# Kernel optimization log

Hardware: AMD Instinct MI355X
Metric: run time of the kernel (lower is better)

The kernel has to match this reference:

```python
import jax, jax.numpy as jnp
import numpy as np

# dims
B, N, L = 8, 128, 512          # batch, n_vars, context_window
PL, ST = 16, 8                  # patch_len, stride
PN = (L - PL) // ST + 1         # patch_num = 63
DM, H, DFF, NL = 128, 16, 256, 2
DK = DM // H
DG, MP, BETA = 8, 3, 0.05       # d_gcn, mp_layers, propbeta
TW = 96                         # target_window


def setup_inputs() -> dict:
    key = jax.random.key(0)
    ks = iter(jax.random.split(key, 64))
    def nrm(shape, s=0.02):
        return jax.random.normal(next(ks), shape, jnp.float32) * s
    inp = {
        "x": jax.random.normal(next(ks), (B, N, L), jnp.float32),
        "adj_logits": jax.random.normal(next(ks), (B, L, N, N), jnp.float32),
        # DGCN params
        "dgcn_start_w": nrm((1, DG)), "dgcn_start_b": jnp.zeros((DG,), jnp.float32),
        "dgcn_mlp_w": nrm(((MP + 1) * DG, 1)), "dgcn_mlp_b": jnp.zeros((1,), jnp.float32),
        # patch embedding + positional
        "W_P": nrm((PL, DM)), "b_P": jnp.zeros((DM,), jnp.float32), "W_pos": nrm((PN, DM)),
        # encoder layers (stacked over NL)
        "Wq": nrm((NL, DM, DM)), "bq": jnp.zeros((NL, DM), jnp.float32),
        "Wk": nrm((NL, DM, DM)), "bk": jnp.zeros((NL, DM), jnp.float32),
        "Wv": nrm((NL, DM, DM)), "bv": jnp.zeros((NL, DM), jnp.float32),
        "Wo": nrm((NL, DM, DM)), "bo": jnp.zeros((NL, DM), jnp.float32),
        "scale": jnp.full((NL,), DK ** -0.5, jnp.float32),
        "bn1_g": jnp.ones((NL, DM), jnp.float32), "bn1_b": jnp.zeros((NL, DM), jnp.float32),
        "ff_w1": nrm((NL, DM, DFF)), "ff_b1": jnp.zeros((NL, DFF), jnp.float32),
        "ff_w2": nrm((NL, DFF, DM)), "ff_b2": jnp.zeros((NL, DM), jnp.float32),
        "bn2_g": jnp.ones((NL, DM), jnp.float32), "bn2_b": jnp.zeros((NL, DM), jnp.float32),
        # head
        "head_w": nrm((DM * PN, TW)), "head_b": jnp.zeros((TW,), jnp.float32),
    }
    return inp


def _bn(x, g, b):
    # BatchNorm1d in training mode over (batch, seq) per feature channel
    mu = x.mean(axis=(0, 1))
    var = x.var(axis=(0, 1))
    return (x - mu) * jax.lax.rsqrt(var + 1e-5) * g + b


def reference(x, adj_logits, dgcn_start_w, dgcn_start_b, dgcn_mlp_w, dgcn_mlp_b,
              W_P, b_P, W_pos, Wq, bq, Wk, bk, Wv, bv, Wo, bo, scale,
              bn1_g, bn1_b, ff_w1, ff_b1, ff_w2, ff_b2, bn2_g, bn2_b,
              head_w, head_b):
    # ---- DGCN: multi-hop diffusion over variables, per time step ----
    x4 = x[..., None]                                   # [b,n,s,1]
    A = jax.nn.softmax(adj_logits, axis=2)              # [b,s,n,m], normalized over source n
    a = jnp.transpose(A, (0, 2, 3, 1))                  # [b,n,m,s]
    h = x4 @ dgcn_start_w + dgcn_start_b                # [b,n,s,d_gcn]
    outs = [h]
    for _ in range(MP):
        h = BETA * x4 + (1.0 - BETA) * jnp.einsum('bnsc,bnms->bmsc', h, a)
        outs.append(h)
    y = (jnp.concatenate(outs, axis=-1) @ dgcn_mlp_w + dgcn_mlp_b)[..., 0]  # [b,n,s]
    # ---- patching ----
    win = jnp.arange(PN)[:, None] * ST + jnp.arange(PL)[None, :]
    z = y[:, :, win]                                    # [b,n,pn,pl]
    # ---- TSTiEncoder (channel independent) ----
    src = (z @ W_P + b_P).reshape(B * N, PN, DM) + W_pos
    prev = None
    for l in range(NL):
        q = (src @ Wq[l] + bq[l]).reshape(-1, PN, H, DK).transpose(0, 2, 1, 3)
        k = (src @ Wk[l] + bk[l]).reshape(-1, PN, H, DK).transpose(0, 2, 1, 3)
        v = (src @ Wv[l] + bv[l]).reshape(-1, PN, H, DK).transpose(0, 2, 1, 3)
        scores = jnp.einsum('bhqd,bhkd->bhqk', q, k) * scale[l]
        if prev is not None:
            scores = scores + prev                      # residual attention
        w = jax.nn.softmax(scores, axis=-1)
        o = jnp.einsum('bhqk,bhkd->bhqd', w, v).transpose(0, 2, 1, 3).reshape(-1, PN, DM)
        src = _bn(src + (o @ Wo[l] + bo[l]), bn1_g[l], bn1_b[l])
        ff = jax.nn.gelu(src @ ff_w1[l] + ff_b1[l], approximate=False) @ ff_w2[l] + ff_b2[l]
        src = _bn(src + ff, bn2_g[l], bn2_b[l])
        prev = scores
    # ---- Flatten_Head ----
    enc = src.reshape(B, N, PN, DM).transpose(0, 1, 3, 2).reshape(B, N, DM * PN)
    return enc @ head_w + head_b                        # [b, n_vars, target_window]
```

## Files before the change

### kernel.cpp

```cpp
#include <hip/hip_runtime.h>
#include <hip/hip_bf16.h>
#include <math.h>

#define RM 64512

typedef short short8 __attribute__((ext_vector_type(8)));
typedef float f32x4 __attribute__((ext_vector_type(4)));
typedef unsigned short ushort4v __attribute__((ext_vector_type(4)));
typedef unsigned short ushort8v __attribute__((ext_vector_type(8)));

__device__ __forceinline__ float gelu_f(float v) {
    return 0.5f * v * (1.0f + erff(v * 0.70710678118654752f));
}
__device__ __forceinline__ float b2f(unsigned short u) {
    unsigned int x = ((unsigned int)u) << 16;
    return __builtin_bit_cast(float, x);
}
__device__ __forceinline__ unsigned short f2b(float f) {
    __hip_bfloat16 h = __float2bfloat16(f);
    return __builtin_bit_cast(unsigned short, h);
}

__global__ __launch_bounds__(256) void wprep_kernel(
    const float* __restrict__ Wq, const float* __restrict__ Wk, const float* __restrict__ Wv,
    const float* __restrict__ Wo, const float* __restrict__ fw1, const float* __restrict__ fw2,
    const float* __restrict__ bq, const float* __restrict__ bk, const float* __restrict__ bv,
    unsigned short* __restrict__ WB, float* __restrict__ bcat)
{
    const int id = blockIdx.y;
    const int l = id / 6, mat = id % 6;
    const float* src; int K, N; size_t off = (size_t)l * 131072;
    switch (mat) {
        case 0: src = Wq  + l*16384; K = 128; N = 128; off += 0;      break;
        case 1: src = Wk  + l*16384; K = 128; N = 128; off += 16384;  break;
        case 2: src = Wv  + l*16384; K = 128; N = 128; off += 32768;  break;
        case 3: src = Wo  + l*16384; K = 128; N = 128; off += 49152;  break;
        case 4: src = fw1 + l*32768; K = 128; N = 256; off += 65536;  break;
        default:src = fw2 + l*32768; K = 256; N = 128; off += 98304;  break;
    }
    const int total = K * N;
    const int ksh = (K == 256) ? 8 : 7;
    for (int idx = blockIdx.x*256 + threadIdx.x; idx < total; idx += gridDim.x*256) {
        int n = idx >> ksh, k = idx & (K - 1);
        WB[off + idx] = f2b(src[(size_t)k*N + n]);
    }
    if (id == 0 && blockIdx.x == 0) {
        for (int idx = threadIdx.x; idx < 768; idx += 256) {
            int ll = idx / 384, j = idx % 384;
            float vv;
            if (j < 128)      vv = bq[ll*128 + j];
            else if (j < 256) vv = bk[ll*128 + j - 128];
            else              vv = bv[ll*128 + j - 256];
            bcat[idx] = vv;
        }
    }
}

__global__ __launch_bounds__(256) void dgcn_kernel(
    const float* __restrict__ x, const float* __restrict__ adj,
    const float* __restrict__ sw, const float* __restrict__ sb,
    const float* __restrict__ mw, const float* __restrict__ mb,
    float* __restrict__ y)
{
    __shared__ __align__(16) unsigned short ET[128*128];
    __shared__ __align__(16) unsigned short hT[16*128];
    __shared__ float red[256];
    __shared__ float iv[128];
    __shared__ float xc[128];
    __shared__ float yac[128];
    const int bid = blockIdx.x;
    const int b = bid >> 9, s = bid & 511;
    const int t = threadIdx.x;
    const int lane = t & 63, wid = t >> 6;
    const float* ap = adj + (size_t)bid * 16384;

    if (t < 128) xc[t] = x[((size_t)b*128 + t)*512 + s];

    {
        const int m = t & 127, ng = t >> 7;
        float sm = 0.f;
        for (int p = 0; p < 16; ++p) {
            const int n0 = p*8 + ng*4;
            float e0 = __expf(ap[(size_t)(n0+0)*128 + m]);
            float e1 = __expf(ap[(size_t)(n0+1)*128 + m]);
            float e2 = __expf(ap[(size_t)(n0+2)*128 + m]);
            float e3 = __expf(ap[(size_t)(n0+3)*128 + m]);
            sm += e0 + e1 + e2 + e3;
            ushort4v u4; u4[0]=f2b(e0); u4[1]=f2b(e1); u4[2]=f2b(e2); u4[3]=f2b(e3);
            *(ushort4v*)((char*)ET + m*256 + (((n0>>3) ^ (m & 15))*16) + (n0 & 7)*2) = u4;
        }
        red[ng*128 + m] = sm;
        *(ushort4v*)&hT[8*128 + t*4] = (ushort4v){0,0,0,0};
    }
    __syncthreads();
    if (t < 128) iv[t] = 1.f / (red[t] + red[128 + t]);
    if (t < 128) {
        const int m = t;
        const float xm = xc[m];
        float yp = 0.f;
        #pragma unroll
        for (int c = 0; c < 8; ++c) {
            float h = xm*sw[c] + sb[c];
            yp += h*mw[c];
            *(unsigned short*)((char*)hT + c*256 + ((((m>>3) ^ c))*16) + (m & 7)*2) = f2b(h);
        }
        yac[m] = yp;
    }
    __syncthreads();

    const int rl = lane & 15, kh = lane >> 4;
    short8 af[2][4];
    float xr[2][4], ivr[2][4];
    #pragma unroll
    for (int ti = 0; ti < 2; ++ti) {
        const int mrow = (wid*2 + ti)*16 + rl;
        #pragma unroll
        for (int ks = 0; ks < 4; ++ks) {
            const int ch = (ks*4 + kh) ^ (mrow & 15);
            af[ti][ks] = *(const short8*)((const char*)ET + mrow*256 + ch*16);
        }
        #pragma unroll
        for (int r = 0; r < 4; ++r) {
            const int m = (wid*2 + ti)*16 + kh*4 + r;
            xr[ti][r]  = 0.05f * xc[m];
            ivr[ti][r] = 0.95f * iv[m];
        }
    }
    float yl[2][4] = {};
    #pragma unroll
    for (int step = 1; step <= 3; ++step) {
        short8 bfr[4];
        #pragma unroll
        for (int ks = 0; ks < 4; ++ks) {
            const int ch = (ks*4 + kh) ^ rl;
            bfr[ks] = *(const short8*)((const char*)hT + rl*256 + ch*16);
        }
        f32x4 acc[2] = {};
        #pragma unroll
        for (int ti = 0; ti < 2; ++ti)
            #pragma unroll
            for (int ks = 0; ks < 4; ++ks)
                acc[ti] = __builtin_amdgcn_mfma_f32_16x16x32_bf16(af[ti][ks], bfr[ks], acc[ti], 0, 0, 0);
        __syncthreads();
        const float mwc = (rl < 8) ? mw[step*8 + rl] : 0.f;
        #pragma unroll
        for (int ti = 0; ti < 2; ++ti) {
            const int m0 = (wid*2 + ti)*16 + kh*4;
            ushort4v hw4;
            float hnew[4];
            #pragma unroll
            for (int r = 0; r < 4; ++r) {
                float v = xr[ti][r] + ivr[ti][r]*acc[ti][r];
                hnew[r] = v;
                hw4[r] = f2b(v);
            }
            *(ushort4v*)((char*)hT + rl*256 + (((m0>>3) ^ rl)*16) + (m0 & 7)*2) = hw4;
            #pragma unroll
            for (int r = 0; r < 4; ++r) {
                float vv = hnew[r]*mwc;
                vv += __shfl_xor(vv, 1);
                vv += __shfl_xor(vv, 2);
                vv += __shfl_xor(vv, 4);
                vv += __shfl_xor(vv, 8);
                yl[ti][r] += vv;
            }
        }
        __syncthreads();
    }
    if (rl == 0) {
        #pragma unroll
        for (int ti = 0; ti < 2; ++ti)
            #pragma unroll
            for (int r = 0; r < 4; ++r)
                yac[(wid*2 + ti)*16 + kh*4 + r] += yl[ti][r];
    }
    __syncthreads();
    if (t < 128) y[((size_t)b*128 + t)*512 + s] = yac[t] + mb[0];
}

__global__ __launch_bounds__(256) void patch_kernel(
    const float* __restrict__ y, const float* __restrict__ Wp, const float* __restrict__ bp,
    const float* __restrict__ Wpos, unsigned short* __restrict__ srcb)
{
    __shared__ float ys[512];
    __shared__ float wps[16*128];
    const int bn = blockIdx.x;
    const int t = threadIdx.x;
    ys[t]       = y[(size_t)bn*512 + t];
    ys[t + 256] = y[(size_t)bn*512 + t + 256];
    #pragma unroll
    for (int r = 0; r < 8; ++r) wps[t + r*256] = Wp[t + r*256];
    __syncthreads();
    for (int cu = t; cu < 1008; cu += 256) {
        int p = cu >> 4, d0 = (cu & 15) * 8;
        float o[8];
        #pragma unroll
        for (int j = 0; j < 8; ++j) o[j] = bp[d0+j] + Wpos[p*128 + d0 + j];
        #pragma unroll
        for (int tt = 0; tt < 16; ++tt) {
            float a = ys[p*8 + tt];
            #pragma unroll
            for (int j = 0; j < 8; ++j) o[j] += a * wps[tt*128 + d0 + j];
        }
        size_t row = (size_t)bn*63 + p;
        ushort8v u;
        #pragma unroll
        for (int j = 0; j < 8; ++j) u[j] = f2b(o[j]);
        *(ushort8v*)&srcb[row*128 + d0] = u;
    }
}

template<int ACT, int OM, int RESMODE, bool STATS, bool AHM, int NB, int KK>
__global__ __launch_bounds__(256) void mgemm(
    const unsigned short* __restrict__ A, const unsigned short* __restrict__ WB,
    const float* __restrict__ bias, const unsigned short* __restrict__ Rsd,
    const float* __restrict__ snR,
    unsigned short* __restrict__ Cb,
    float* __restrict__ part)
{
    constexpr int NTOT = NB * 128;
    constexpr int kch = KK >> 3;
    constexpr int KT = KK >> 7;
    __shared__ __align__(16) unsigned short AsL[128*128];
    __shared__ __align__(16) unsigned short BsL[128*128];
    __shared__ float sred[4][16][8], qred[4][16][8];
    const int t = threadIdx.x;
    const int lane = t & 63, wid = t >> 6;
    const int wr = wid >> 1, wc = wid & 1;
    const int m0 = blockIdx.x * 128;
    const int kh = lane >> 4, rl = lane & 15;
    float sj[8] = {}, qj[8] = {};

    for (int ib = 0; ib < NB; ++ib) {
        f32x4 acc[4][4] = {};
        for (int kt = 0; kt < KT; ++kt) {
            if (ib == 0 || KT > 1) {
                #pragma unroll
                for (int i = 0; i < 8; ++i) {
                    int cid = i*256 + t;
                    int row = cid >> 4, c = cid & 15;
                    int c_g = c ^ (row & 7);
                    const unsigned short* ga;
                    if constexpr (AHM) ga = A + ((size_t)c_g*RM + (m0+row))*8;
                    else               ga = A + ((size_t)(m0+row)*kch + kt*16 + c_g)*8;
                    __builtin_amdgcn_global_load_lds((const unsigned int*)ga,
                        (unsigned int*)&AsL[(i*256 + wid*64)*8], 16, 0, 0);
                }
            }
            #pragma unroll
            for (int i = 0; i < 8; ++i) {
                int cid = i*256 + t;
                int nr = cid >> 4, c = cid & 15;
                const unsigned short* gb = WB + (size_t)ib*128*KK
                    + ((size_t)nr*kch + kt*16 + (c ^ (nr & 7)))*8;
                __builtin_amdgcn_global_load_lds((const unsigned int*)gb,
                    (unsigned int*)&BsL[(i*256 + wid*64)*8], 16, 0, 0);
            }
            __syncthreads();
            #pragma unroll
            for (int ks = 0; ks < 4; ++ks) {
                const int cA = ks*4 + kh;
                short8 af[4], bfr[4];
                #pragma unroll
                for (int i = 0; i < 4; ++i) {
                    int row = wr*64 + i*16 + rl;
                    af[i]  = *(const short8*)&AsL[row*128 + ((cA ^ (row & 7))*8)];
                    int cn  = wc*64 + i*16 + rl;
                    bfr[i] = *(const short8*)&BsL[cn*128 + ((cA ^ (cn & 7))*8)];
                }
                #pragma unroll
                for (int i = 0; i < 4; ++i)
                    #pragma unroll
                    for (int j = 0; j < 4; ++j)
                        acc[i][j] = __builtin_amdgcn_mfma_f32_16x16x32_bf16(af[i], bfr[j], acc[i][j], 0, 0, 0);
            }
            __syncthreads();
        }
        #pragma unroll
        for (int j = 0; j < 4; ++j) {
            const int col_l = wc*64 + j*16 + rl;
            const float bs = bias[ib*128 + col_l];
            const int chunk = col_l >> 3, bo2 = (col_l & 7) << 1;
            #pragma unroll
            for (int i = 0; i < 4; ++i) {
                #pragma unroll
                for (int r = 0; r < 4; ++r) {
                    const int row_l = wr*64 + i*16 + (lane>>4)*4 + r;
                    float v = acc[i][j][r] + bs;
                    if constexpr (ACT == 1) v = gelu_f(v);
                    *(unsigned short*)((char*)BsL + row_l*256 + ((chunk ^ (row_l & 15))<<4) + bo2) = f2b(v);
                }
            }
        }
        __syncthreads();
        if constexpr (OM == 1) {
            #pragma unroll
            for (int it = 0; it < 8; ++it) {
                int cid = it*256 + t;
                int row_l = cid & 127, hd_l = cid >> 7;
                ushort8v u = *(const ushort8v*)((const char*)BsL + row_l*256 + ((hd_l ^ (row_l & 15))<<4));
                *(ushort8v*)&Cb[(((size_t)(ib*16 + hd_l))*RM + m0 + row_l)*8] = u;
            }
        } else {
            #pragma unroll
            for (int it = 0; it < 8; ++it) {
                const int row_l = it*16 + (t >> 4), c = t & 15;
                ushort8v u = *(const ushort8v*)((const char*)BsL + row_l*256 + ((c ^ (row_l & 15))<<4));
                const size_t gbase = (size_t)(m0 + row_l)*NTOT + ib*128 + c*8;
                ushort8v rs = {};
                if constexpr (RESMODE != 0) rs = *(const ushort8v*)&Rsd[gbase];
                ushort8v o8;
                #pragma unroll
                for (int jj = 0; jj < 8; ++jj) {
                    float v = b2f(u[jj]);
                    if constexpr (RESMODE == 1) v += b2f(rs[jj]);
                    if constexpr (RESMODE == 2) v += b2f(rs[jj])*snR[c*8+jj] + snR[128 + c*8 + jj];
                    if constexpr (STATS) { sj[jj] += v; qj[jj] += v*v; }
                    o8[jj] = f2b(v);
                }
                *(ushort8v*)&Cb[gbase] = o8;
            }
        }
        __syncthreads();
    }
    if constexpr (STATS) {
        #pragma unroll
        for (int jj = 0; jj < 8; ++jj) {
            sj[jj] += __shfl_xor(sj[jj], 16); qj[jj] += __shfl_xor(qj[jj], 16);
            sj[jj] += __shfl_xor(sj[jj], 32); qj[jj] += __shfl_xor(qj[jj], 32);
        }
        if ((lane >> 4) == 0) {
            #pragma unroll
            for (int jj = 0; jj < 8; ++jj) {
                sred[wid][lane][jj] = sj[jj];
                qred[wid][lane][jj] = qj[jj];
            }
        }
        __syncthreads();
        if (t < 128) {
            const int c2 = t >> 3, jj = t & 7;
            float s = sred[0][c2][jj] + sred[1][c2][jj] + sred[2][c2][jj] + sred[3][c2][jj];
            float q = qred[0][c2][jj] + qred[1][c2][jj] + qred[2][c2][jj] + qred[3][c2][jj];
            part[(size_t)blockIdx.x*256 + t]       = s;
            part[(size_t)blockIdx.x*256 + 128 + t] = q;
        }
    }
}

__global__ __launch_bounds__(256) void bnred(const float* __restrict__ part,
    const float* __restrict__ g, const float* __restrict__ b, float* __restrict__ sn)
{
    const int c = blockIdx.x, t = threadIdx.x;
    float s = 0.f, q = 0.f;
    for (int bid = t; bid < 504; bid += 256) {
        s += part[(size_t)bid*256 + c];
        q += part[(size_t)bid*256 + 128 + c];
    }
    __shared__ float ls[256], lq[256];
    ls[t] = s; lq[t] = q;
    __syncthreads();
    for (int o = 128; o > 0; o >>= 1) {
        if (t < o) { ls[t] += ls[t+o]; lq[t] += lq[t+o]; }
        __syncthreads();
    }
    if (t == 0) {
        const float invM = 1.f / (float)RM;
        float mean = ls[0] * invM;
        float var  = fmaxf(lq[0]*invM - mean*mean, 0.f);
        float sc = g[c] * rsqrtf(var + 1e-5f);
        sn[c]       = sc;
        sn[128 + c] = b[c] - mean*sc;
    }
}

__global__ __launch_bounds__(256) void wfold(const unsigned short* __restrict__ WBs,
    const float* __restrict__ sn, const float* __restrict__ bsrc,
    unsigned short* __restrict__ WBd, float* __restrict__ bdst)
{
    const int t = threadIdx.x, wv = t >> 6, lane = t & 63;
    const int n = blockIdx.x*4 + wv;
    float w1 = b2f(WBs[(size_t)n*128 + lane]);
    float w2 = b2f(WBs[(size_t)n*128 + 64 + lane]);
    WBd[(size_t)n*128 + lane]      = f2b(sn[lane]*w1);
    WBd[(size_t)n*128 + 64 + lane] = f2b(sn[64+lane]*w2);
    float bacc = sn[128+lane]*w1 + sn[192+lane]*w2;
    #pragma unroll
    for (int msk = 1; msk < 64; msk <<= 1) bacc += __shfl_xor(bacc, msk);
    if (lane == 0) bdst[n] = bsrc[n] + bacc;
}

__global__ __launch_bounds__(64) void attn_kernel(
    const unsigned short* __restrict__ qkv, const unsigned short* __restrict__ qkvP,
    const float* __restrict__ scale, const int l, unsigned short* __restrict__ ob)
{
    __shared__ float ks[504], vs[504], k0s[504];
    const int bn = blockIdx.x, hd = blockIdx.y;
    const int t = threadIdx.x;
    const size_t rbase = (size_t)hd*RM + (size_t)bn*63;
    if (t < 63) {
        ushort8v ku = *(const ushort8v*)&qkv[((size_t)16*RM*8) + (rbase + t)*8];
        ushort8v vu = *(const ushort8v*)&qkv[((size_t)32*RM*8) + (rbase + t)*8];
        #pragma unroll
        for (int d = 0; d < 8; ++d) { ks[t*8+d] = b2f(ku[d]); vs[t*8+d] = b2f(vu[d]); }
        if (l > 0) {
            ushort8v k0u = *(const ushort8v*)&qkvP[((size_t)16*RM*8) + (rbase + t)*8];
            #pragma unroll
            for (int d = 0; d < 8; ++d) k0s[t*8+d] = b2f(k0u[d]);
        }
    }
    float qr[8] = {}, q0r[8] = {};
    if (t < 63) {
        ushort8v qu = *(const ushort8v*)&qkv[(rbase + t)*8];
        #pragma unroll
        for (int d = 0; d < 8; ++d) qr[d] = b2f(qu[d]);
        if (l > 0) {
            ushort8v q0u = *(const ushort8v*)&qkvP[(rbase + t)*8];
            #pragma unroll
            for (int d = 0; d < 8; ++d) q0r[d] = b2f(q0u[d]);
        }
    }
    __syncthreads();
    if (t >= 63) return;
    const float scl  = scale[l];
    const float scl0 = (l > 0) ? scale[0] : 0.f;
    float mr = 0.f, sum = 0.f;
    float oa[8] = {};
    for (int j = 0; j < 63; ++j) {
        float s = 0.f;
        #pragma unroll
        for (int d = 0; d < 8; ++d) s += qr[d]*ks[j*8+d];
        s *= scl;
        if (l > 0) {
            float s0 = 0.f;
            #pragma unroll
            for (int d = 0; d < 8; ++d) s0 += q0r[d]*k0s[j*8+d];
            s += scl0 * s0;
        }
        if (j == 0) {
            mr = s; sum = 1.f;
            #pragma unroll
            for (int d = 0; d < 8; ++d) oa[d] = vs[d];
        } else if (s > mr + 8.f) {
            float c = __expf(mr - s);
            sum = sum*c + 1.f;
            #pragma unroll
            for (int d = 0; d < 8; ++d) oa[d] = oa[d]*c + vs[j*8+d];
            mr = s;
        } else {
            float p = __expf(s - mr);
            sum += p;
            #pragma unroll
            for (int d = 0; d < 8; ++d) oa[d] += p*vs[j*8+d];
        }
    }
    float inv = 1.f / sum;
    ushort8v u;
    #pragma unroll
    for (int d = 0; d < 8; ++d) u[d] = f2b(oa[d]*inv);
    *(ushort8v*)&ob[((size_t)hd*RM + (size_t)bn*63 + t)*8] = u;
}

__global__ __launch_bounds__(256) void hwfold(
    const float* __restrict__ hw, const float* __restrict__ hb,
    const float* __restrict__ sn,
    unsigned short* __restrict__ hwTf, float* __restrict__ hbf)
{
    const int n = blockIdx.x;
    const int t = threadIdx.x;
    float bacc = 0.f;
    if (n < 96) {
        for (int idx = t; idx < 8192; idx += 256) {
            int ksv = idx >> 8, kl = idx & 255;
            unsigned short w = 0;
            if (kl < 252) {
                int k = ksv*252 + kl;
                int d = (int)(((unsigned)k * 33289u) >> 21);
                float wv = hw[(size_t)k*96 + n];
                w = f2b(sn[d] * wv);
                bacc += sn[128 + d] * wv;
            }
            hwTf[(size_t)(ksv*128 + n)*256 + kl] = w;
        }
    } else {
        for (int idx = t; idx < 8192; idx += 256) {
            int ksv = idx >> 8, kl = idx & 255;
            hwTf[(size_t)(ksv*128 + n)*256 + kl] = 0;
        }
    }
    __shared__ float ls[256];
    ls[t] = bacc;
    __syncthreads();
    for (int o = 128; o > 0; o >>= 1) { if (t < o) ls[t] += ls[t+o]; __syncthreads(); }
    if (t == 0 && n < 96) hbf[n] = hb[n] + ls[0];
}

__global__ __launch_bounds__(256) void mhead(
    const unsigned short* __restrict__ A, const unsigned short* __restrict__ BW,
    float* __restrict__ part)
{
    __shared__ __align__(16) unsigned short AsL[128*128];
    __shared__ __align__(16) unsigned short BsL[128*128];
    const int t = threadIdx.x;
    const int lane = t & 63, wid = t >> 6;
    const int wr = wid >> 1, wc = wid & 1;
    const int m0 = blockIdx.x * 128;
    const int ks = blockIdx.y;
    f32x4 acc[4][3] = {};
    for (int kt = 0; kt < 2; ++kt) {
        #pragma unroll
        for (int i = 0; i < 8; ++i) {
            int cid = i*256 + t;
            int nr = cid >> 4, c = cid & 15;
            const unsigned short* gb = BW + ((size_t)(ks*128 + nr)*256 + kt*128 + ((c ^ (nr & 7))*8));
            __builtin_amdgcn_global_load_lds((const unsigned int*)gb,
                (unsigned int*)&BsL[(i*256 + wid*64)*8], 16, 0, 0);
        }
        #pragma unroll
        for (int i = 0; i < 8; ++i) {
            int cid = i*256 + t;
            int row = cid >> 4, c_lds = cid & 15;
            int c_g = c_lds ^ (row & 7);
            int kl0 = kt*128 + c_g*8;
            ushort8v u;
            #pragma unroll
            for (int j = 0; j < 8; ++j) {
                int kl = kl0 + j;
                if (kl < 252) {
                    int dl = (kl*521) >> 15;
                    int p  = kl - dl*63;
                    u[j] = A[((size_t)(m0+row)*63 + p)*128 + ks*4 + dl];
                } else u[j] = 0;
            }
            *(ushort8v*)&AsL[cid*8] = u;
        }
        __syncthreads();
        const int kh = lane >> 4, rl = lane & 15;
        #pragma unroll
        for (int kq = 0; kq < 4; ++kq) {
            const int cA = kq*4 + kh;
            short8 af[4], bfr[3];
            #pragma unroll
            for (int i = 0; i < 4; ++i) {
                int row = wr*64 + i*16 + rl;
                af[i] = *(const short8*)&AsL[row*128 + ((cA ^ (row & 7))*8)];
            }
            #pragma unroll
            for (int j = 0; j < 3; ++j) {
                int cn = wc*48 + j*16 + rl;
                bfr[j] = *(const short8*)&BsL[cn*128 + ((cA ^ (cn & 7))*8)];
            }
            #pragma unroll
            for (int i = 0; i < 4; ++i)
                #pragma unroll
                for (int j = 0; j < 3; ++j)
                    acc[i][j] = __builtin_amdgcn_mfma_f32_16x16x32_bf16(af[i], bfr[j], acc[i][j], 0, 0, 0);
        }
        __syncthreads();
    }
    const int rl = lane & 15, rq = lane >> 4;
    #pragma unroll
    for (int j = 0; j < 3; ++j) {
        const int col = wc*48 + j*16 + rl;
        #pragma unroll
        for (int i = 0; i < 4; ++i) {
            const int rbase = m0 + wr*64 + i*16 + rq*4;
            #pragma unroll
            for (int r = 0; r < 4; ++r)
                part[((size_t)ks*1024 + rbase + r)*96 + col] = acc[i][j][r];
        }
    }
}

__global__ __launch_bounds__(256) void head_reduce(const float* __restrict__ part,
    const float* __restrict__ hbf, float* __restrict__ out)
{
    int idx = blockIdx.x*256 + threadIdx.x;
    float s = hbf[idx % 96];
    #pragma unroll
    for (int blk = 0; blk < 32; ++blk) s += part[(size_t)blk*98304 + idx];
    out[idx] = s;
}

extern "C" void kernel_launch(void* const* d_in, const int* in_sizes, int n_in,
                              void* d_out, int out_size, void* d_ws, size_t ws_size,
                              hipStream_t stream) {
    const float* x    = (const float*)d_in[0];
    const float* adj  = (const float*)d_in[1];
    const float* sw   = (const float*)d_in[2];
    const float* sb   = (const float*)d_in[3];
    const float* mw   = (const float*)d_in[4];
    const float* mb   = (const float*)d_in[5];
    const float* Wp   = (const float*)d_in[6];
    const float* bp   = (const float*)d_in[7];
    const float* Wpos = (const float*)d_in[8];
    const float* Wq   = (const float*)d_in[9];
    const float* bq   = (const float*)d_in[10];
    const float* Wk   = (const float*)d_in[11];
    const float* bk   = (const float*)d_in[12];
    const float* Wv   = (const float*)d_in[13];
    const float* bv   = (const float*)d_in[14];
    const float* Wo   = (const float*)d_in[15];
    const float* bo   = (const float*)d_in[16];
    const float* scale= (const float*)d_in[17];
    const float* bn1g = (const float*)d_in[18];
    const float* bn1b = (const float*)d_in[19];
    const float* fw1  = (const float*)d_in[20];
    const float* fb1  = (const float*)d_in[21];
    const float* fw2  = (const float*)d_in[22];
    const float* fb2  = (const float*)d_in[23];
    const float* bn2g = (const float*)d_in[24];
    const float* bn2b = (const float*)d_in[25];
    const float* hw   = (const float*)d_in[26];
    const float* hb   = (const float*)d_in[27];
    float* out = (float*)d_out;

    float* y     = (float*)d_ws;
    float* part  = y     + 524288;
    float* snorm = part  + 129024;
    float* bcat  = snorm + 1024;
    float* bfold = bcat  + 768;
    float* hbf   = bfold + 1024;
    float* hpart = hbf   + 128;
    unsigned short* srcb = (unsigned short*)(hpart + 3145728);
    unsigned short* t1b  = srcb + 8257536;
    unsigned short* t2b  = t1b  + 8257536;
    unsigned short* g    = t2b  + 8257536;
    unsigned short* o_bf = g    + 16515072;
    unsigned short* qkv0 = o_bf + 8257536;
    unsigned short* qkv1 = qkv0 + 24772608;
    unsigned short* WB   = qkv1 + 24772608;
    unsigned short* WF   = WB   + 262144;
    unsigned short* hwTf = WF   + 131072;

    wprep_kernel<<<dim3(64,12), 256, 0, stream>>>(Wq, Wk, Wv, Wo, fw1, fw2, bq, bk, bv, WB, bcat);
    dgcn_kernel<<<4096, 256, 0, stream>>>(x, adj, sw, sb, mw, mb, y);
    patch_kernel<<<1024, 256, 0, stream>>>(y, Wp, bp, Wpos, srcb);

    mgemm<0,1,0,false,false,3,128><<<504, 256, 0, stream>>>(srcb, WB, bcat, nullptr, nullptr, qkv0, nullptr);
    attn_kernel<<<dim3(1024,16), 64, 0, stream>>>(qkv0, qkv0, scale, 0, o_bf);
    mgemm<0,2,1,true,true,1,128><<<504, 256, 0, stream>>>(o_bf, WB + 49152, bo, srcb, nullptr, t1b, part);
    bnred<<<128, 256, 0, stream>>>(part, bn1g, bn1b, snorm);
    wfold<<<64, 256, 0, stream>>>(WB + 65536, snorm, fb1, WF, bfold);
    mgemm<1,2,0,false,false,2,128><<<504, 256, 0, stream>>>(t1b, WF, bfold, nullptr, nullptr, g, nullptr);
    mgemm<0,2,2,true,false,1,256><<<504, 256, 0, stream>>>(g, WB + 98304, fb2, t1b, snorm, t2b, part);
    bnred<<<128, 256, 0, stream>>>(part, bn2g, bn2b, snorm + 256);
    wfold<<<96, 256, 0, stream>>>(WB + 131072, snorm + 256, bcat + 384, WF + 65536, bfold + 512);

    mgemm<0,1,0,false,false,3,128><<<504, 256, 0, stream>>>(t2b, WF + 65536, bfold + 512, nullptr, nullptr, qkv1, nullptr);
    attn_kernel<<<dim3(1024,16), 64, 0, stream>>>(qkv1, qkv0, scale, 1, o_bf);
    mgemm<0,2,2,true,true,1,128><<<504, 256, 0, stream>>>(o_bf, WB + 131072 + 49152, bo + 128, t2b, snorm + 256, t1b, part);
    bnred<<<128, 256, 0, stream>>>(part, bn1g + 128, bn1b + 128, snorm + 512);
    wfold<<<64, 256, 0, stream>>>(WB + 131072 + 65536, snorm + 512, fb1 + 256, WF + 32768, bfold + 256);
    mgemm<1,2,0,false,false,2,128><<<504, 256, 0, stream>>>(t1b, WF + 32768, bfold + 256, nullptr, nullptr, g, nullptr);
    mgemm<0,2,2,true,false,1,256><<<504, 256, 0, stream>>>(g, WB + 131072 + 98304, fb2 + 128, t1b, snorm + 512, t2b, part);
    bnred<<<128, 256, 0, stream>>>(part, bn2g + 128, bn2b + 128, snorm + 768);

    hwfold<<<128, 256, 0, stream>>>(hw, hb, snorm + 768, hwTf, hbf);
    mhead<<<dim3(8,32), 256, 0, stream>>>(t2b, hwTf, hpart);
    head_reduce<<<384, 256, 0, stream>>>(hpart, hbf, out);
}
```

Measured before the change: 431.1 us.

## Fuse feed-forward GEMMs into one kernel and pack four heads per attention block

Adds an ffused kernel that runs FF1 with GELU, keeps the 128x256 intermediate in LDS, and then runs FF2 plus the residual add and BatchNorm partial sums in the same kernel. This removes the global round trip of the g buffer and one launch per layer. Separately, attn_kernel now handles four heads per 256-thread block instead of one head per 64-thread block, which cuts the block count and launch overhead. The fused kernel uses about 128KB of LDS, so occupancy is limited to one block per CU and global loads are less overlapped with compute.

```diff
diff --git a/kernel.cpp b/kernel.cpp
--- a/kernel.cpp
+++ b/kernel.cpp
@@ -347,6 +347,183 @@
     }
 }
 
+__global__ __launch_bounds__(256) void ffused(
+    const unsigned short* __restrict__ A, const unsigned short* __restrict__ W1,
+    const float* __restrict__ b1, const unsigned short* __restrict__ W2,
+    const float* __restrict__ b2, const unsigned short* __restrict__ Rsd,
+    const float* __restrict__ snR,
+    unsigned short* __restrict__ Cb, float* __restrict__ part)
+{
+    __shared__ __align__(16) unsigned short AsL[128*128];
+    __shared__ __align__(16) unsigned short BsL[128*128];
+    __shared__ __align__(16) unsigned short G[128*256];
+    __shared__ float sred[4][16][8], qred[4][16][8];
+    const int t = threadIdx.x;
+    const int lane = t & 63, wid = t >> 6;
+    const int wr = wid >> 1, wc = wid & 1;
+    const int m0 = blockIdx.x * 128;
+    const int kh = lane >> 4, rl = lane & 15;
+
+    #pragma unroll
+    for (int i = 0; i < 8; ++i) {
+        int cid = i*256 + t;
+        int row = cid >> 4, c = cid & 15;
+        const unsigned short* ga = A + ((size_t)(m0+row)*16 + (c ^ (row & 7)))*8;
+        __builtin_amdgcn_global_load_lds((const unsigned int*)ga,
+            (unsigned int*)&AsL[(i*256 + wid*64)*8], 16, 0, 0);
+    }
+    #pragma unroll
+    for (int i = 0; i < 8; ++i) {
+        int cid = i*256 + t;
+        int nr = cid >> 4, c = cid & 15;
+        const unsigned short* gb = W1 + ((size_t)nr*16 + (c ^ (nr & 7)))*8;
+        __builtin_amdgcn_global_load_lds((const unsigned int*)gb,
+            (unsigned int*)&BsL[(i*256 + wid*64)*8], 16, 0, 0);
+    }
+    __syncthreads();
+    for (int ib = 0; ib < 2; ++ib) {
+        f32x4 acc[4][4] = {};
+        #pragma unroll
+        for (int ks = 0; ks < 4; ++ks) {
+            const int cA = ks*4 + kh;
+            short8 af[4], bfr[4];
+            #pragma unroll
+            for (int i = 0; i < 4; ++i) {
+                int row = wr*64 + i*16 + rl;
+                af[i]  = *(const short8*)&AsL[row*128 + ((cA ^ (row & 7))*8)];
+                int cn  = wc*64 + i*16 + rl;
+                bfr[i] = *(const short8*)&BsL[cn*128 + ((cA ^ (cn & 7))*8)];
+            }
+            #pragma unroll
+            for (int i = 0; i < 4; ++i)
+                #pragma unroll
+                for (int j = 0; j < 4; ++j)
+                    acc[i][j] = __builtin_amdgcn_mfma_f32_16x16x32_bf16(af[i], bfr[j], acc[i][j], 0, 0, 0);
+        }
+        __syncthreads();
+        if (ib == 0) {
+            #pragma unroll
+            for (int i = 0; i < 8; ++i) {
+                int cid = i*256 + t;
+                int nr = cid >> 4, c = cid & 15;
+                const unsigned short* gb = W1 + ((size_t)(128+nr)*16 + (c ^ (nr & 7)))*8;
+                __builtin_amdgcn_global_load_lds((const unsigned int*)gb,
+                    (unsigned int*)&BsL[(i*256 + wid*64)*8], 16, 0, 0);
+            }
+        }
+        #pragma unroll
+        for (int j = 0; j < 4; ++j) {
+            const int col_l = wc*64 + j*16 + rl;
+            const int colg = ib*128 + col_l;
+            const float bs = b1[colg];
+            const int cg = colg >> 3, bo2 = (colg & 7) << 1;
+            #pragma unroll
+            for (int i = 0; i < 4; ++i) {
+                #pragma unroll
+                for (int r = 0; r < 4; ++r) {
+                    const int row_l = wr*64 + i*16 + (lane>>4)*4 + r;
+                    float v = gelu_f(acc[i][j][r] + bs);
+                    *(unsigned short*)((char*)G + row_l*512 + (((cg ^ (row_l & 15)))<<4) + bo2) = f2b(v);
+                }
+            }
+        }
+        __syncthreads();
+    }
+    f32x4 acc2[4][4] = {};
+    for (int kt = 0; kt < 2; ++kt) {
+        if (kt == 1) {
+            #pragma unroll
+            for (int i = 0; i < 8; ++i) {
+                int cid = i*256 + t;
+                int nr = cid >> 4, c = cid & 15;
+                const unsigned short* gb = W2 + ((size_t)nr*32 + 16 + (c ^ (nr & 7)))*8;
+                __builtin_amdgcn_global_load_lds((const unsigned int*)gb,
+                    (unsigned int*)&BsL[(i*256 + wid*64)*8], 16, 0, 0);
+            }
+        } else {
+            #pragma unroll
+            for (int i = 0; i < 8; ++i) {
+                int cid = i*256 + t;
+                int nr = cid >> 4, c = cid & 15;
+                const unsigned short* gb = W2 + ((size_t)nr*32 + (c ^ (nr & 7)))*8;
+                __builtin_amdgcn_global_load_lds((const unsigned int*)gb,
+                    (unsigned int*)&BsL[(i*256 + wid*64)*8], 16, 0, 0);
+            }
+        }
+        __syncthreads();
+        #pragma unroll
+        for (int ks = 0; ks < 4; ++ks) {
+            const int cA = ks*4 + kh;
+            short8 af[4], bfr[4];
+            #pragma unroll
+            for (int i = 0; i < 4; ++i) {
+                int row = wr*64 + i*16 + rl;
+                af[i] = *(const short8*)((const char*)G + row*512 + ((((kt*16 + cA) ^ (row & 15)))<<4));
+                int cn  = wc*64 + i*16 + rl;
+                bfr[i] = *(const short8*)&BsL[cn*128 + ((cA ^ (cn & 7))*8)];
+            }
+            #pragma unroll
+            for (int i = 0; i < 4; ++i)
+                #pragma unroll
+                for (int j = 0; j < 4; ++j)
+                    acc2[i][j] = __builtin_amdgcn_mfma_f32_16x16x32_bf16(af[i], bfr[j], acc2[i][j], 0, 0, 0);
+        }
+        __syncthreads();
+    }
+    #pragma unroll
+    for (int j = 0; j < 4; ++j) {
+        const int col_l = wc*64 + j*16 + rl;
+        const float bs = b2[col_l];
+        const int chunk = col_l >> 3, bo2 = (col_l & 7) << 1;
+        #pragma unroll
+        for (int i = 0; i < 4; ++i) {
+            #pragma unroll
+            for (int r = 0; r < 4; ++r) {
+                const int row_l = wr*64 + i*16 + (lane>>4)*4 + r;
+                *(unsigned short*)((char*)AsL + row_l*256 + ((chunk ^ (row_l & 15))<<4) + bo2)
+                    = f2b(acc2[i][j][r] + bs);
+            }
+        }
+    }
+    __syncthreads();
+    float sj[8] = {}, qj[8] = {};
+    #pragma unroll
+    for (int it = 0; it < 8; ++it) {
+        const int row_l = it*16 + (t >> 4), c = t & 15;
+        ushort8v u = *(const ushort8v*)((const char*)AsL + row_l*256 + ((c ^ (row_l & 15))<<4));
+        const size_t gbase = (size_t)(m0 + row_l)*128 + c*8;
+        ushort8v rs = *(const ushort8v*)&Rsd[gbase];
+        ushort8v o8;
+        #pragma unroll
+        for (int jj = 0; jj < 8; ++jj) {
+            float v = b2f(u[jj]) + b2f(rs[jj])*snR[c*8+jj] + snR[128 + c*8 + jj];
+            sj[jj] += v; qj[jj] += v*v;
+            o8[jj] = f2b(v);
+        }
+        *(ushort8v*)&Cb[gbase] = o8;
+    }
+    #pragma unroll
+    for (int jj = 0; jj < 8; ++jj) {
+        sj[jj] += __shfl_xor(sj[jj], 16); qj[jj] += __shfl_xor(qj[jj], 16);
+        sj[jj] += __shfl_xor(sj[jj], 32); qj[jj] += __shfl_xor(qj[jj], 32);
+    }
+    if ((lane >> 4) == 0) {
+        #pragma unroll
+        for (int jj = 0; jj < 8; ++jj) {
+            sred[wid][lane][jj] = sj[jj];
+            qred[wid][lane][jj] = qj[jj];
+        }
+    }
+    __syncthreads();
+    if (t < 128) {
+        const int c2 = t >> 3, jj = t & 7;
+        float s = sred[0][c2][jj] + sred[1][c2][jj] + sred[2][c2][jj] + sred[3][c2][jj];
+        float q = qred[0][c2][jj] + qred[1][c2][jj] + qred[2][c2][jj] + qred[3][c2][jj];
+        part[(size_t)blockIdx.x*256 + t]       = s;
+        part[(size_t)blockIdx.x*256 + 128 + t] = q;
+    }
+}
+
 __global__ __launch_bounds__(256) void bnred(const float* __restrict__ part,
     const float* __restrict__ g, const float* __restrict__ b, float* __restrict__ sn)
 {
@@ -389,38 +566,35 @@
     if (lane == 0) bdst[n] = bsrc[n] + bacc;
 }
 
-__global__ __launch_bounds__(64) void attn_kernel(
+__global__ __launch_bounds__(256) void attn_kernel(
     const unsigned short* __restrict__ qkv, const unsigned short* __restrict__ qkvP,
     const float* __restrict__ scale, const int l, unsigned short* __restrict__ ob)
 {
-    __shared__ float ks[504], vs[504], k0s[504];
-    const int bn = blockIdx.x, hd = blockIdx.y;
-    const int t = threadIdx.x;
+    __shared__ float ks[4][504], vs[4][504], k0s[4][504];
+    const int bn = blockIdx.x;
+    const int t = threadIdx.x, wid = t >> 6, lane = t & 63;
+    const int hd = blockIdx.y*4 + wid;
     const size_t rbase = (size_t)hd*RM + (size_t)bn*63;
-    if (t < 63) {
-        ushort8v ku = *(const ushort8v*)&qkv[((size_t)16*RM*8) + (rbase + t)*8];
-        ushort8v vu = *(const ushort8v*)&qkv[((size_t)32*RM*8) + (rbase + t)*8];
-        #pragma unroll
-        for (int d = 0; d < 8; ++d) { ks[t*8+d] = b2f(ku[d]); vs[t*8+d] = b2f(vu[d]); }
-        if (l > 0) {
-            ushort8v k0u = *(const ushort8v*)&qkvP[((size_t)16*RM*8) + (rbase + t)*8];
-            #pragma unroll
-            for (int d = 0; d < 8; ++d) k0s[t*8+d] = b2f(k0u[d]);
-        }
-    }
     float qr[8] = {}, q0r[8] = {};
-    if (t < 63) {
-        ushort8v qu = *(const ushort8v*)&qkv[(rbase + t)*8];
+    if (lane < 63) {
+        ushort8v ku = *(const ushort8v*)&qkv[((size_t)16*RM*8) + (rbase + lane)*8];
+        ushort8v vu = *(const ushort8v*)&qkv[((size_t)32*RM*8) + (rbase + lane)*8];
+        #pragma unroll
+        for (int d = 0; d < 8; ++d) { ks[wid][lane*8+d] = b2f(ku[d]); vs[wid][lane*8+d] = b2f(vu[d]); }
+        ushort8v qu = *(const ushort8v*)&qkv[(rbase + lane)*8];
         #pragma unroll
         for (int d = 0; d < 8; ++d) qr[d] = b2f(qu[d]);
         if (l > 0) {
-            ushort8v q0u = *(const ushort8v*)&qkvP[(rbase + t)*8];
+            ushort8v k0u = *(const ushort8v*)&qkvP[((size_t)16*RM*8) + (rbase + lane)*8];
+            #pragma unroll
+            for (int d = 0; d < 8; ++d) k0s[wid][lane*8+d] = b2f(k0u[d]);
+            ushort8v q0u = *(const ushort8v*)&qkvP[(rbase + lane)*8];
             #pragma unroll
             for (int d = 0; d < 8; ++d) q0r[d] = b2f(q0u[d]);
         }
     }
     __syncthreads();
-    if (t >= 63) return;
+    if (lane >= 63) return;
     const float scl  = scale[l];
     const float scl0 = (l > 0) ? scale[0] : 0.f;
     float mr = 0.f, sum = 0.f;
@@ -428,36 +602,36 @@
     for (int j = 0; j < 63; ++j) {
         float s = 0.f;
         #pragma unroll
-        for (int d = 0; d < 8; ++d) s += qr[d]*ks[j*8+d];
+        for (int d = 0; d < 8; ++d) s += qr[d]*ks[wid][j*8+d];
         s *= scl;
         if (l > 0) {
             float s0 = 0.f;
             #pragma unroll
-            for (int d = 0; d < 8; ++d) s0 += q0r[d]*k0s[j*8+d];
+            for (int d = 0; d < 8; ++d) s0 += q0r[d]*k0s[wid][j*8+d];
             s += scl0 * s0;
         }
         if (j == 0) {
             mr = s; sum = 1.f;
             #pragma unroll
-            for (int d = 0; d < 8; ++d) oa[d] = vs[d];
+            for (int d = 0; d < 8; ++d) oa[d] = vs[wid][d];
         } else if (s > mr + 8.f) {
             float c = __expf(mr - s);
             sum = sum*c + 1.f;
             #pragma unroll
-            for (int d = 0; d < 8; ++d) oa[d] = oa[d]*c + vs[j*8+d];
+            for (int d = 0; d < 8; ++d) oa[d] = oa[d]*c + vs[wid][j*8+d];
             mr = s;
         } else {
             float p = __expf(s - mr);
             sum += p;
             #pragma unroll
-            for (int d = 0; d < 8; ++d) oa[d] += p*vs[j*8+d];
+            for (int d = 0; d < 8; ++d) oa[d] += p*vs[wid][j*8+d];
         }
     }
     float inv = 1.f / sum;
     ushort8v u;
     #pragma unroll
     for (int d = 0; d < 8; ++d) u[d] = f2b(oa[d]*inv);
-    *(ushort8v*)&ob[((size_t)hd*RM + (size_t)bn*63 + t)*8] = u;
+    *(ushort8v*)&ob[((size_t)hd*RM + (size_t)bn*63 + lane)*8] = u;
 }
 
 __global__ __launch_bounds__(256) void hwfold(
@@ -637,22 +811,20 @@
     patch_kernel<<<1024, 256, 0, stream>>>(y, Wp, bp, Wpos, srcb);
 
     mgemm<0,1,0,false,false,3,128><<<504, 256, 0, stream>>>(srcb, WB, bcat, nullptr, nullptr, qkv0, nullptr);
-    attn_kernel<<<dim3(1024,16), 64, 0, stream>>>(qkv0, qkv0, scale, 0, o_bf);
+    attn_kernel<<<dim3(1024,4), 256, 0, stream>>>(qkv0, qkv0, scale, 0, o_bf);
     mgemm<0,2,1,true,true,1,128><<<504, 256, 0, stream>>>(o_bf, WB + 49152, bo, srcb, nullptr, t1b, part);
     bnred<<<128, 256, 0, stream>>>(part, bn1g, bn1b, snorm);
     wfold<<<64, 256, 0, stream>>>(WB + 65536, snorm, fb1, WF, bfold);
-    mgemm<1,2,0,false,false,2,128><<<504, 256, 0, stream>>>(t1b, WF, bfold, nullptr, nullptr, g, nullptr);
-    mgemm<0,2,2,true,false,1,256><<<504, 256, 0, stream>>>(g, WB + 98304, fb2, t1b, snorm, t2b, part);
+    ffused<<<504, 256, 0, stream>>>(t1b, WF, bfold, WB + 98304, fb2, t1b, snorm, t2b, part);
     bnred<<<128, 256, 0, stream>>>(part, bn2g, bn2b, snorm + 256);
     wfold<<<96, 256, 0, stream>>>(WB + 131072, snorm + 256, bcat + 384, WF + 65536, bfold + 512);
 
     mgemm<0,1,0,false,false,3,128><<<504, 256, 0, stream>>>(t2b, WF + 65536, bfold + 512, nullptr, nullptr, qkv1, nullptr);
-    attn_kernel<<<dim3(1024,16), 64, 0, stream>>>(qkv1, qkv0, scale, 1, o_bf);
+    attn_kernel<<<dim3(1024,4), 256, 0, stream>>>(qkv1, qkv0, scale, 1, o_bf);
     mgemm<0,2,2,true,true,1,128><<<504, 256, 0, stream>>>(o_bf, WB + 131072 + 49152, bo + 128, t2b, snorm + 256, t1b, part);
     bnred<<<128, 256, 0, stream>>>(part, bn1g + 128, bn1b + 128, snorm + 512);
     wfold<<<64, 256, 0, stream>>>(WB + 131072 + 65536, snorm + 512, fb1 + 256, WF + 32768, bfold + 256);
-    mgemm<1,2,0,false,false,2,128><<<504, 256, 0, stream>>>(t1b, WF + 32768, bfold + 256, nullptr, nullptr, g, nullptr);
-    mgemm<0,2,2,true,false,1,256><<<504, 256, 0, stream>>>(g, WB + 131072 + 98304, fb2 + 128, t1b, snorm + 512, t2b, part);
+    ffused<<<504, 256, 0, stream>>>(t1b, WF + 32768, bfold + 256, WB + 131072 + 98304, fb2 + 128, t1b, snorm + 512, t2b, part);
     bnred<<<128, 256, 0, stream>>>(part, bn2g + 128, bn2b + 128, snorm + 768);
 
     hwfold<<<128, 256, 0, stream>>>(hw, hb, snorm + 768, hwTf, hbf);
```

New measurement: 438.3 us. Within noise of the previous version (+1.7%).
